# Optimization experiments

Measured on AMD Instinct MI355X. Metric: run time of the kernel, lower is better.

Reference implementation:

```python
import jax, jax.numpy as jnp
import numpy as np

N_NODES = 100000


def setup_inputs() -> dict:
    key = jax.random.key(0)
    k1, k2, k3, k4, k5 = jax.random.split(key, 5)
    d_in, d_out, n_edges = 128, 128, 640000
    x = jax.random.normal(k1, (N_NODES, d_in), dtype=jnp.float32)
    edge_index = jax.random.randint(k2, (2, n_edges), 0, N_NODES, dtype=jnp.int64)
    # uniform(size, W) in the source is U(-1/sqrt(in), 1/sqrt(in)); scaled normal is fine as data
    s = 1.0 / np.sqrt(d_in)
    Wc = jax.random.normal(k3, (d_in, d_out), dtype=jnp.float32) * s
    Wn = jax.random.normal(k4, (d_in, d_out), dtype=jnp.float32) * s
    b = jax.random.normal(k5, (d_out,), dtype=jnp.float32) * s
    return {"x": x, "edge_index": edge_index, "Wc": Wc, "Wn": Wn, "b": b}


def reference(x, edge_index, Wc, Wn, b):
    row, col = edge_index[0], edge_index[1]
    alpha = x @ Wc                      # [N, out]
    beta = x @ Wn                       # [N, out]
    # Vectorized scatter-mean replacing the original per-node Python loop:
    # gamma[n] = mean(beta[col[row == n]])
    num = jax.ops.segment_sum(beta[col], row, num_segments=N_NODES)   # [N, out]
    cnt = jax.ops.segment_sum(jnp.ones_like(row, dtype=beta.dtype), row, num_segments=N_NODES)
    gamma = num / jnp.maximum(cnt, 1.0)[:, None]  # NOTE: unused below, exactly as in the original forward
    del gamma
    # The original returns alpha + beta + bias (gamma is dead code in the source).
    return alpha + beta + b
```

## Files before the change

kernel.cpp:

```cpp
#include <hip/hip_runtime.h>
#include <hip/hip_bf16.h>


#define NROWS 100000

typedef __attribute__((ext_vector_type(8))) __bf16 bf16x8;
typedef __attribute__((ext_vector_type(4))) float f32x4;

__device__ __forceinline__ bf16x8 pack8(const float4 lo, const float4 hi) {
    bf16x8 r;
    r[0] = (__bf16)lo.x; r[1] = (__bf16)lo.y; r[2] = (__bf16)lo.z; r[3] = (__bf16)lo.w;
    r[4] = (__bf16)hi.x; r[5] = (__bf16)hi.y; r[6] = (__bf16)hi.z; r[7] = (__bf16)hi.w;
    return r;
}

__global__ void prep_wt(const float* __restrict__ Wc, const float* __restrict__ Wn,
                        __bf16* __restrict__ wt) {
    int i = blockIdx.x * 256 + threadIdx.x;
    int n = i >> 7, k = i & 127;
    wt[i] = (__bf16)(Wc[k * 128 + n] + Wn[k * 128 + n]);
}

__global__ __launch_bounds__(256) void gemm_bias(
    const float* __restrict__ x, const __bf16* __restrict__ wt,
    const float* __restrict__ bias_g, float* __restrict__ out) {

    __shared__ __align__(16) __bf16 sWt[128 * 136];

    const int tid  = threadIdx.x;
    const int wave = tid >> 6;
    const int lane = tid & 63;
    const int quad = lane >> 4;
    const int l16  = lane & 15;

    const long rowbase = (long)blockIdx.x * 128 + wave * 32;
    const bool valid = rowbase < NROWS;

    bf16x8 xb[2][4];
    if (valid) {
        const float* xr0 = x + (rowbase + l16) * 128;
        const float* xr1 = xr0 + 16 * 128;
        #pragma unroll
        for (int kc = 0; kc < 4; ++kc) {
            const int ko = kc * 32 + quad * 8;
            xb[0][kc] = pack8(*(const float4*)(xr0 + ko), *(const float4*)(xr0 + ko + 4));
            xb[1][kc] = pack8(*(const float4*)(xr1 + ko), *(const float4*)(xr1 + ko + 4));
        }
    }

    #pragma unroll
    for (int it = 0; it < 8; ++it) {
        int idx8 = it * 256 + tid;
        int n = idx8 >> 4;
        int k = (idx8 & 15) << 3;
        *(bf16x8*)&sWt[n * 136 + k] = *(const bf16x8*)(wt + (idx8 << 3));
    }
    __syncthreads();
    if (!valid) return;

    f32x4 bv[8];
    #pragma unroll
    for (int ct = 0; ct < 8; ++ct)
        bv[ct] = *(const f32x4*)(bias_g + ct * 16 + quad * 4);

    f32x4 acc[2][8] = {};
    #pragma unroll
    for (int kc = 0; kc < 4; ++kc) {
        const int ko = kc * 32 + quad * 8;
        #pragma unroll
        for (int ct = 0; ct < 8; ++ct) {
            bf16x8 wa = *(const bf16x8*)&sWt[(ct * 16 + l16) * 136 + ko];
            acc[0][ct] = __builtin_amdgcn_mfma_f32_16x16x32_bf16(wa, xb[0][kc], acc[0][ct], 0, 0, 0);
            acc[1][ct] = __builtin_amdgcn_mfma_f32_16x16x32_bf16(wa, xb[1][kc], acc[1][ct], 0, 0, 0);
        }
    }

    #pragma unroll
    for (int g = 0; g < 2; ++g) {
        float* orow = out + (rowbase + g * 16 + l16) * 128 + quad * 4;
        #pragma unroll
        for (int ct = 0; ct < 8; ++ct) {
            f32x4 v = acc[g][ct] + bv[ct];
            __builtin_nontemporal_store(v, (f32x4*)(orow + ct * 16));
        }
    }
}

extern "C" void kernel_launch(void* const* d_in, const int* in_sizes, int n_in,
                              void* d_out, int out_size, void* d_ws, size_t ws_size,
                              hipStream_t stream) {
    const float* x  = (const float*)d_in[0];
    const float* Wc = (const float*)d_in[2];
    const float* Wn = (const float*)d_in[3];
    const float* b  = (const float*)d_in[4];
    __bf16* wt = (__bf16*)d_ws;
    float* out = (float*)d_out;

    prep_wt<<<64, 256, 0, stream>>>(Wc, Wn, wt);
    const int nblocks = (NROWS + 127) / 128;
    gemm_bias<<<nblocks, 256, 0, stream>>>(x, wt, b, out);
}
```

Before: 117.3 us.

## Load pre-swizzled bf16 weights directly from global, dropping LDS staging

The weight-prep kernel now writes the combined bf16 weights in the exact per-lane fragment order the MFMA loop consumes. The GEMM kernel reads them straight from global memory (L2/L1-cached) instead of staging 34KB into LDS behind a barrier. This removes the LDS copy and __syncthreads and allows more blocks per CU via launch bounds. x loads become nontemporal. The cost is repeated global/L1 weight fetches per wave instead of shared LDS reuse.

```diff
diff --git a/kernel.cpp b/kernel.cpp
--- a/kernel.cpp
+++ b/kernel.cpp
@@ -7,25 +7,32 @@
 typedef __attribute__((ext_vector_type(8))) __bf16 bf16x8;
 typedef __attribute__((ext_vector_type(4))) float f32x4;
 
-__device__ __forceinline__ bf16x8 pack8(const float4 lo, const float4 hi) {
+__device__ __forceinline__ bf16x8 pack8(const f32x4 lo, const f32x4 hi) {
     bf16x8 r;
-    r[0] = (__bf16)lo.x; r[1] = (__bf16)lo.y; r[2] = (__bf16)lo.z; r[3] = (__bf16)lo.w;
-    r[4] = (__bf16)hi.x; r[5] = (__bf16)hi.y; r[6] = (__bf16)hi.z; r[7] = (__bf16)hi.w;
+    r[0] = (__bf16)lo[0]; r[1] = (__bf16)lo[1]; r[2] = (__bf16)lo[2]; r[3] = (__bf16)lo[3];
+    r[4] = (__bf16)hi[0]; r[5] = (__bf16)hi[1]; r[6] = (__bf16)hi[2]; r[7] = (__bf16)hi[3];
     return r;
 }
 
 __global__ void prep_wt(const float* __restrict__ Wc, const float* __restrict__ Wn,
-                        __bf16* __restrict__ wt) {
-    int i = blockIdx.x * 256 + threadIdx.x;
-    int n = i >> 7, k = i & 127;
-    wt[i] = (__bf16)(Wc[k * 128 + n] + Wn[k * 128 + n]);
+                        __bf16* __restrict__ wtL) {
+    int t = blockIdx.x * 256 + threadIdx.x;
+    int n = t & 127;
+    int oct = t >> 7;
+    int ct = n >> 4, l16 = n & 15;
+    int kc = oct >> 2, quad = oct & 3;
+    bf16x8 v;
+    #pragma unroll
+    for (int j = 0; j < 8; ++j) {
+        int k = (oct << 3) + j;
+        v[j] = (__bf16)(Wc[k * 128 + n] + Wn[k * 128 + n]);
+    }
+    *(bf16x8*)&wtL[(((ct * 4 + kc) * 16 + l16) * 4 + quad) * 8] = v;
 }
 
-__global__ __launch_bounds__(256) void gemm_bias(
-    const float* __restrict__ x, const __bf16* __restrict__ wt,
+__global__ __launch_bounds__(256, 3) void gemm_bias(
+    const float* __restrict__ x, const __bf16* __restrict__ wtL,
     const float* __restrict__ bias_g, float* __restrict__ out) {
-
-    __shared__ __align__(16) __bf16 sWt[128 * 136];
 
     const int tid  = threadIdx.x;
     const int wave = tid >> 6;
@@ -34,29 +41,23 @@
     const int l16  = lane & 15;
 
     const long rowbase = (long)blockIdx.x * 128 + wave * 32;
-    const bool valid = rowbase < NROWS;
+    if (rowbase >= NROWS) return;
 
     bf16x8 xb[2][4];
-    if (valid) {
-        const float* xr0 = x + (rowbase + l16) * 128;
-        const float* xr1 = xr0 + 16 * 128;
+    {
+        const f32x4* xr0 = (const f32x4*)(x + (rowbase + l16) * 128);
+        const f32x4* xr1 = (const f32x4*)(x + (rowbase + 16 + l16) * 128);
         #pragma unroll
         for (int kc = 0; kc < 4; ++kc) {
-            const int ko = kc * 32 + quad * 8;
-            xb[0][kc] = pack8(*(const float4*)(xr0 + ko), *(const float4*)(xr0 + ko + 4));
-            xb[1][kc] = pack8(*(const float4*)(xr1 + ko), *(const float4*)(xr1 + ko + 4));
+            const int q4 = kc * 8 + quad * 2;
+            f32x4 lo0 = __builtin_nontemporal_load(xr0 + q4);
+            f32x4 hi0 = __builtin_nontemporal_load(xr0 + q4 + 1);
+            f32x4 lo1 = __builtin_nontemporal_load(xr1 + q4);
+            f32x4 hi1 = __builtin_nontemporal_load(xr1 + q4 + 1);
+            xb[0][kc] = pack8(lo0, hi0);
+            xb[1][kc] = pack8(lo1, hi1);
         }
     }
-
-    #pragma unroll
-    for (int it = 0; it < 8; ++it) {
-        int idx8 = it * 256 + tid;
-        int n = idx8 >> 4;
-        int k = (idx8 & 15) << 3;
-        *(bf16x8*)&sWt[n * 136 + k] = *(const bf16x8*)(wt + (idx8 << 3));
-    }
-    __syncthreads();
-    if (!valid) return;
 
     f32x4 bv[8];
     #pragma unroll
@@ -64,12 +65,12 @@
         bv[ct] = *(const f32x4*)(bias_g + ct * 16 + quad * 4);
 
     f32x4 acc[2][8] = {};
+    const __bf16* wf = wtL + l16 * 32 + quad * 8;
     #pragma unroll
     for (int kc = 0; kc < 4; ++kc) {
-        const int ko = kc * 32 + quad * 8;
         #pragma unroll
         for (int ct = 0; ct < 8; ++ct) {
-            bf16x8 wa = *(const bf16x8*)&sWt[(ct * 16 + l16) * 136 + ko];
+            bf16x8 wa = *(const bf16x8*)(wf + (ct * 4 + kc) * 512);
             acc[0][ct] = __builtin_amdgcn_mfma_f32_16x16x32_bf16(wa, xb[0][kc], acc[0][ct], 0, 0, 0);
             acc[1][ct] = __builtin_amdgcn_mfma_f32_16x16x32_bf16(wa, xb[1][kc], acc[1][ct], 0, 0, 0);
         }
@@ -93,10 +94,10 @@
     const float* Wc = (const float*)d_in[2];
     const float* Wn = (const float*)d_in[3];
     const float* b  = (const float*)d_in[4];
-    __bf16* wt = (__bf16*)d_ws;
+    __bf16* wtL = (__bf16*)d_ws;
     float* out = (float*)d_out;
 
-    prep_wt<<<64, 256, 0, stream>>>(Wc, Wn, wt);
+    prep_wt<<<8, 256, 0, stream>>>(Wc, Wn, wtL);
     const int nblocks = (NROWS + 127) / 128;
-    gemm_bias<<<nblocks, 256, 0, stream>>>(x, wt, b, out);
+    gemm_bias<<<nblocks, 256, 0, stream>>>(x, wtL, b, out);
 }
```

After: 128.7 us. 1.1x slower.
